# Kernel tuning notes

Hardware: AMD Instinct MI355X
Metric: run time of the kernel (lower is better)

The kernel has to match this reference:

```python
import jax, jax.numpy as jnp
import numpy as np

B, T, C = 4, 2048, 1024
H = 16
HS = C // H  # 64

def setup_inputs() -> dict:
    key = jax.random.key(0)
    k1, k2, k3, k4 = jax.random.split(key, 4)
    scale = 0.02
    return {
        "x": jax.random.normal(k1, (B, T, C), dtype=jnp.float32),
        "w_kqv": jax.random.normal(k2, (C, 3 * C), dtype=jnp.float32) * scale,
        "w_proj": jax.random.normal(k3, (C, C), dtype=jnp.float32) * scale,
        "b_proj": jax.random.normal(k4, (C,), dtype=jnp.float32) * scale,
    }

def reference(x, w_kqv, w_proj, b_proj):
    b, t, c = x.shape
    qkv = x @ w_kqv                       # [B,T,3C]
    q, k, v = jnp.split(qkv, 3, axis=-1)
    def heads(a):
        return a.reshape(b, t, H, HS).transpose(0, 2, 1, 3)  # [B,H,T,HS]
    q, k, v = heads(q), heads(k), heads(v)
    # faithful to source: scores MULTIPLIED by sqrt(head_size)
    scores = jnp.einsum('bhqd,bhkd->bhqk', q, k) * (HS ** 0.5)
    mask = jnp.tril(jnp.ones((t, t), dtype=bool))
    scores = jnp.where(mask[None, None], scores, -jnp.inf)
    attn = jax.nn.softmax(scores, axis=-1)
    out = jnp.einsum('bhqk,bhkd->bhqd', attn, v)  # [B,H,T,HS]
    out = out.transpose(0, 2, 1, 3).reshape(b, t, c)
    return out @ w_proj + b_proj
```

## Files before the change

kernel.cpp:

```cpp
#include <hip/hip_runtime.h>
#include <hip/hip_bf16.h>
#include <cstdint>

#define BB 4
#define TT 2048
#define CC 1024
#define HH 16
#define HS 64
#define MM (BB*TT)

#define QSCALE 11.5415603629f

typedef _Float16 f16;
typedef _Float16 f16x8 __attribute__((ext_vector_type(8)));
typedef _Float16 f16x4 __attribute__((ext_vector_type(4)));
typedef float f32x4 __attribute__((ext_vector_type(4)));
typedef float f32x16 __attribute__((ext_vector_type(16)));

#define MFMA16(a,b,c) __builtin_amdgcn_mfma_f32_16x16x32_f16(a,b,c,0,0,0)
#define MFMA32(a,b,c) __builtin_amdgcn_mfma_f32_32x32x16_f16(a,b,c,0,0,0)

__device__ __forceinline__ void g2lds16(void* lds, const void* g) {
  __builtin_amdgcn_global_load_lds(
      (const __attribute__((address_space(1))) void*)g,
      (__attribute__((address_space(3))) void*)lds, 16, 0, 0);
}

__device__ __forceinline__ int pk2(float a, float b) {
  auto r = __builtin_amdgcn_cvt_pkrtz(a, b);
  return __builtin_bit_cast(int, r);
}

union U8 { int4 i; f16x8 h; };

__global__ __launch_bounds__(256) void cvt_kernel(const float* __restrict__ in,
                                                  f16* __restrict__ out, int n4) {
  int i = blockIdx.x * blockDim.x + threadIdx.x;
  if (i < n4) {
    float4 v = ((const float4*)in)[i];
    f16x4 o;
    o[0] = (f16)v.x; o[1] = (f16)v.y; o[2] = (f16)v.z; o[3] = (f16)v.w;
    ((f16x4*)out)[i] = o;
  }
}

__global__ __launch_bounds__(256) void transpose_cvt(const float* __restrict__ in,
                                                     f16* __restrict__ out,
                                                     int K, int N) {
  __shared__ float tile[32][33];
  int n0 = blockIdx.x * 32, k0 = blockIdx.y * 32;
  int tx = threadIdx.x, ty = threadIdx.y;
  #pragma unroll
  for (int i = 0; i < 32; i += 8)
    tile[ty + i][tx] = in[(size_t)(k0 + ty + i) * N + n0 + tx];
  __syncthreads();
  #pragma unroll
  for (int i = 0; i < 32; i += 8)
    out[(size_t)(n0 + ty + i) * K + k0 + tx] = (f16)tile[tx][ty + i];
}

__device__ __forceinline__ void gstage(const f16* __restrict__ A,
                                       const f16* __restrict__ Bt,
                                       f16* as, f16* bs,
                                       int row0, int col0, int kt, int t) {
  const int K = 1024;
  #pragma unroll
  for (int i = 0; i < 2; ++i) {
    int off = i * 8192 + t * 16;
    int row = off >> 7;
    int cbB = off & 127;
    int scb = cbB ^ ((row & 7) << 4);
    g2lds16((char*)as + off, (const char*)(A  + (size_t)(row0 + row) * K + kt) + scb);
    g2lds16((char*)bs + off, (const char*)(Bt + (size_t)(col0 + row) * K + kt) + scb);
  }
}

template<int EPI>
__global__ __launch_bounds__(512) void gemm_bt(const f16* __restrict__ A,
                                               const f16* __restrict__ Bt,
                                               f16* __restrict__ qT,
                                               f16* __restrict__ kT,
                                               f16* __restrict__ vT,
                                               const float* __restrict__ bias,
                                               float* __restrict__ outF) {
  const int K = 1024;
  __shared__ f16 As[2][128 * 64];
  __shared__ f16 Bs[2][128 * 64];
  const int t = threadIdx.x;
  const int l = t & 63, w = t >> 6;
  const int lr = l & 15, lh = l >> 4;
  const int row0 = blockIdx.y * 128, col0 = blockIdx.x * 128;
  const int wm = w >> 2, wn = w & 3;
  const int wr = wm * 64, wc = wn * 32;
  const int sx = (lr & 7) << 4;

  f32x4 acc[4][2] = {};

  gstage(A, Bt, As[0], Bs[0], row0, col0, 0, t);
  int buf = 0;
  for (int kt = 0; kt < K; kt += 64) {
    asm volatile("" ::: "memory");
    const bool pf = (kt + 64) < K;
    if (pf) gstage(A, Bt, As[buf ^ 1], Bs[buf ^ 1], row0, col0, kt + 64, t);
    if (pf) asm volatile("s_waitcnt vmcnt(4)" ::: "memory");
    else    asm volatile("s_waitcnt vmcnt(0)" ::: "memory");
    __builtin_amdgcn_sched_barrier(0);
    __builtin_amdgcn_s_barrier();
    const char* as = (const char*)As[buf];
    const char* bs = (const char*)Bs[buf];
    __builtin_amdgcn_s_setprio(1);
    #pragma unroll
    for (int kk = 0; kk < 64; kk += 32) {
      f16x8 af[4], bfr[2];
      #pragma unroll
      for (int m = 0; m < 4; ++m)
        af[m]  = *(const f16x8*)(as + (wr + m * 16 + lr) * 128
                                    + ((kk * 2 + lh * 16) ^ sx));
      #pragma unroll
      for (int n = 0; n < 2; ++n)
        bfr[n] = *(const f16x8*)(bs + (wc + n * 16 + lr) * 128
                                    + ((kk * 2 + lh * 16) ^ sx));
      #pragma unroll
      for (int m = 0; m < 4; ++m)
        #pragma unroll
        for (int n = 0; n < 2; ++n)
          acc[m][n] = MFMA16(af[m], bfr[n], acc[m][n]);
    }
    __builtin_amdgcn_s_setprio(0);
    __builtin_amdgcn_sched_barrier(0);
    __builtin_amdgcn_s_barrier();
    buf ^= 1;
  }

  #pragma unroll
  for (int m = 0; m < 4; ++m) {
    #pragma unroll
    for (int n = 0; n < 2; ++n) {
      #pragma unroll
      for (int j = 0; j < 4; ++j) {
        float val = acc[m][n][j];
        int gr = row0 + wr + m * 16 + lh * 4 + j;
        int gc = col0 + wc + n * 16 + lr;
        if (EPI == 0) {
          int which = gc >> 10;
          int c = gc & 1023;
          int h = c >> 6, d = c & 63;
          int b = gr >> 11, tt = gr & 2047;
          size_t bh = (size_t)(b * HH + h);
          if (which == 0)      qT[(bh * TT + tt) * HS + d] = (f16)(val * QSCALE);
          else if (which == 1) kT[(bh * TT + tt) * HS + d] = (f16)val;
          else                 vT[(bh * HS + d) * TT + tt] = (f16)val;
        } else {
          outF[(size_t)gr * CC + gc] = val + bias[gc];
        }
      }
    }
  }
}

template<bool MASKED>
__device__ __forceinline__ void step32L(
    int kglob, int qa, int l31, int hi,
    const f16* __restrict__ ks, const f16* __restrict__ vs, int kbs,
    const f16x8 (&qf)[4],
    float& m, f32x4& lv, f32x16& oA, f32x16& oB) {
  const int sx = (l31 & 7) << 4;
  const char* krow = (const char*)(ks + (kbs + l31) * 64);
  f32x16 s = {};
  #pragma unroll
  for (int j = 0; j < 4; ++j) {
    f16x8 kf = *(const f16x8*)(krow + ((j * 32 + hi * 16) ^ sx));
    s = MFMA32(kf, qf[j], s);
  }
  float p[16];
  #pragma unroll
  for (int r = 0; r < 16; ++r) {
    if (MASKED) {
      int k = kglob + (r & 3) + 8 * (r >> 2) + 4 * hi;
      p[r] = (k <= qa) ? s[r] : -INFINITY;
    } else p[r] = s[r];
  }
  float t0 = fmaxf(fmaxf(p[0], p[1]), fmaxf(p[2], p[3]));
  float t1 = fmaxf(fmaxf(p[4], p[5]), fmaxf(p[6], p[7]));
  float t2 = fmaxf(fmaxf(p[8], p[9]), fmaxf(p[10], p[11]));
  float t3 = fmaxf(fmaxf(p[12], p[13]), fmaxf(p[14], p[15]));
  float mx = fmaxf(fmaxf(t0, t1), fmaxf(t2, t3));
  if (__any(mx > m + 14.0f)) {
    mx = fmaxf(mx, __shfl_xor(mx, 32));
    float mn = fmaxf(m, mx);
    float corr = __builtin_amdgcn_exp2f(m - mn);
    m = mn;
    #pragma unroll
    for (int r = 0; r < 4; ++r) lv[r] *= corr;
    #pragma unroll
    for (int r = 0; r < 16; ++r) { oA[r] *= corr; oB[r] *= corr; }
  }
  #pragma unroll
  for (int r = 0; r < 16; ++r) {
    p[r] = __builtin_amdgcn_exp2f(p[r] - m);
    lv[r & 3] += p[r];
  }
  int pk[8], xk[8];
  #pragma unroll
  for (int j = 0; j < 8; ++j) pk[j] = pk2(p[2 * j], p[2 * j + 1]);
  #pragma unroll
  for (int j = 0; j < 8; ++j) xk[j] = __shfl_xor(pk[j], 32);
  U8 b0, b1;
  b0.i = (int4){ hi ? xk[2] : pk[0], hi ? xk[3] : pk[1],
                 hi ? pk[2] : xk[0], hi ? pk[3] : xk[1] };
  b1.i = (int4){ hi ? xk[6] : pk[4], hi ? xk[7] : pk[5],
                 hi ? pk[6] : xk[4], hi ? pk[7] : xk[5] };
  const char* vrow0 = (const char*)(vs + l31 * 64);
  const char* vrow1 = (const char*)(vs + (l31 + 32) * 64);
  const int kc0 = (kbs * 2 + hi * 16) ^ sx;
  const int kc1 = (kbs * 2 + hi * 16 + 32) ^ sx;
  f16x8 v00 = *(const f16x8*)(vrow0 + kc0);
  f16x8 v01 = *(const f16x8*)(vrow0 + kc1);
  f16x8 v10 = *(const f16x8*)(vrow1 + kc0);
  f16x8 v11 = *(const f16x8*)(vrow1 + kc1);
  oA = MFMA32(v00, b0.h, oA);
  oA = MFMA32(v01, b1.h, oA);
  oB = MFMA32(v10, b0.h, oB);
  oB = MFMA32(v11, b1.h, oB);
}

__device__ __forceinline__ void stage_tile(const f16* __restrict__ Kb,
                                           const f16* __restrict__ Vb,
                                           f16* ks, f16* vs,
                                           int kb, int w, int l) {
  #pragma unroll
  for (int j = 0; j < 2; ++j) {
    int off = w * 2048 + j * 1024 + l * 16;
    int row = off >> 7;
    int cb  = off & 127;
    int scb = cb ^ ((row & 7) << 4);
    g2lds16((char*)ks + off, (const char*)(Kb + (size_t)(kb + row) * HS) + scb);
    g2lds16((char*)vs + off, (const char*)(Vb + (size_t)row * TT + kb) + scb);
  }
}

__global__ __launch_bounds__(256) void attn_kernel(const f16* __restrict__ qT,
                                                   const f16* __restrict__ kT,
                                                   const f16* __restrict__ vT,
                                                   f16* __restrict__ aout) {
  const int bh = blockIdx.x;
  const int pr = blockIdx.y;
  const int t = threadIdx.x, l = t & 63, w = t >> 6;
  const int l31 = l & 31, hi = l >> 5;
  const f16* __restrict__ Qb = qT + (size_t)bh * TT * HS;
  const f16* __restrict__ Kb = kT + (size_t)bh * TT * HS;
  const f16* __restrict__ Vb = vT + (size_t)bh * HS * TT;
  const int b = bh >> 4, h = bh & 15;

  __shared__ f16 Ks[2][64 * 64];
  __shared__ f16 Vs[2][64 * 64];

  #pragma unroll
  for (int ph = 0; ph < 2; ++ph) {
    const int qb = ph ? pr : (15 - pr);
    const int q0w = qb * 128 + w * 32;
    const int qa = q0w + l31;

    f16x8 qf[4];
    #pragma unroll
    for (int j = 0; j < 4; ++j)
      qf[j] = *(const f16x8*)&Qb[(size_t)qa * HS + 16 * j + hi * 8];

    float m = -INFINITY;
    f32x4 lv = {};
    f32x16 oA = {}, oB = {};

    const int nt = 2 * qb + 2;
    stage_tile(Kb, Vb, Ks[0], Vs[0], 0, w, l);
    __syncthreads();
    int buf = 0;
    for (int ti = 0; ti < nt; ++ti) {
      if (ti + 1 < nt)
        stage_tile(Kb, Vb, Ks[buf ^ 1], Vs[buf ^ 1], (ti + 1) * 64, w, l);
      const int kb = ti * 64;
      const f16* ks = Ks[buf];
      const f16* vs = Vs[buf];
      if (kb < q0w)
        step32L<false>(kb, qa, l31, hi, ks, vs, 0, qf, m, lv, oA, oB);
      else if (kb == q0w)
        step32L<true >(kb, qa, l31, hi, ks, vs, 0, qf, m, lv, oA, oB);
      if (kb + 32 < q0w)
        step32L<false>(kb + 32, qa, l31, hi, ks, vs, 32, qf, m, lv, oA, oB);
      else if (kb + 32 == q0w)
        step32L<true >(kb + 32, qa, l31, hi, ks, vs, 32, qf, m, lv, oA, oB);
      __syncthreads();
      buf ^= 1;
    }

    float lsum = (lv[0] + lv[1]) + (lv[2] + lv[3]);
    lsum += __shfl_xor(lsum, 32);
    float li = 1.0f / lsum;

    f16* orow = aout + (size_t)(b * TT + qa) * CC + h * HS;
    #pragma unroll
    for (int rq = 0; rq < 4; ++rq) {
      f16x4 o4a, o4b;
      #pragma unroll
      for (int j = 0; j < 4; ++j) {
        int r = rq * 4 + j;
        o4a[j] = (f16)(oA[r] * li);
        o4b[j] = (f16)(oB[r] * li);
      }
      int dA = 8 * rq + 4 * hi;
      *(f16x4*)&orow[dA]      = o4a;
      *(f16x4*)&orow[32 + dA] = o4b;
    }
    __syncthreads();
  }
}

extern "C" void kernel_launch(void* const* d_in, const int* in_sizes, int n_in,
                              void* d_out, int out_size, void* d_ws, size_t ws_size,
                              hipStream_t stream) {
  const float* x      = (const float*)d_in[0];
  const float* w_kqv  = (const float*)d_in[1];
  const float* w_proj = (const float*)d_in[2];
  const float* b_proj = (const float*)d_in[3];
  float* out = (float*)d_out;

  char* ws = (char*)d_ws;
  f16* xb    = (f16*)(ws);
  f16* wkqvT = (f16*)(ws + 16777216);
  f16* wpT   = (f16*)(ws + 23068672);
  f16* qT    = (f16*)(ws + 25165824);
  f16* kT    = (f16*)(ws + 41943040);
  f16* vT    = (f16*)(ws + 58720256);
  f16* aout  = (f16*)(ws + 75497472);

  cvt_kernel<<<8192, 256, 0, stream>>>(x, xb, (MM * CC) / 4);
  transpose_cvt<<<dim3(3 * CC / 32, CC / 32), dim3(32, 8), 0, stream>>>(w_kqv, wkqvT, CC, 3 * CC);
  transpose_cvt<<<dim3(CC / 32, CC / 32), dim3(32, 8), 0, stream>>>(w_proj, wpT, CC, CC);

  gemm_bt<0><<<dim3(3 * CC / 128, MM / 128), 512, 0, stream>>>(xb, wkqvT, qT, kT, vT, nullptr, nullptr);

  attn_kernel<<<dim3(BB * HH, 8), 256, 0, stream>>>(qT, kT, vT, aout);

  gemm_bt<1><<<dim3(CC / 128, MM / 128), 512, 0, stream>>>(aout, wpT, nullptr, nullptr, nullptr, b_proj, out);
}
```

Before: 211.4 us.

## Halve GEMM K-tile with paired-row LDS layout and split QK^T MFMA chains

The projection GEMM now stages a 32-wide K slice per iteration instead of 64. It uses a new LDS layout that packs two rows per 128-byte line with a different XOR swizzle. This halves LDS use per block, which may allow more blocks per CU, at the cost of twice as many loop iterations and barriers. Separately, the attention QK^T score computation splits its four dependent MFMAs into two independent accumulator chains summed afterwards, to shorten the MFMA dependency chain.

```diff
diff --git a/kernel.cpp b/kernel.cpp
--- a/kernel.cpp
+++ b/kernel.cpp
@@ -64,15 +64,11 @@
                                        f16* as, f16* bs,
                                        int row0, int col0, int kt, int t) {
   const int K = 1024;
-  #pragma unroll
-  for (int i = 0; i < 2; ++i) {
-    int off = i * 8192 + t * 16;
-    int row = off >> 7;
-    int cbB = off & 127;
-    int scb = cbB ^ ((row & 7) << 4);
-    g2lds16((char*)as + off, (const char*)(A  + (size_t)(row0 + row) * K + kt) + scb);
-    g2lds16((char*)bs + off, (const char*)(Bt + (size_t)(col0 + row) * K + kt) + scb);
-  }
+  int off = t * 16;
+  int row = ((off >> 7) << 1) | ((off >> 6) & 1);
+  int cb  = (off & 63) ^ (((off >> 7) & 3) << 4);
+  g2lds16((char*)as + off, (const char*)(A  + (size_t)(row0 + row) * K + kt) + cb);
+  g2lds16((char*)bs + off, (const char*)(Bt + (size_t)(col0 + row) * K + kt) + cb);
 }
 
 template<int EPI>
@@ -84,42 +80,44 @@
                                                const float* __restrict__ bias,
                                                float* __restrict__ outF) {
   const int K = 1024;
-  __shared__ f16 As[2][128 * 64];
-  __shared__ f16 Bs[2][128 * 64];
+  __shared__ f16 As[2][128 * 32];
+  __shared__ f16 Bs[2][128 * 32];
   const int t = threadIdx.x;
   const int l = t & 63, w = t >> 6;
   const int lr = l & 15, lh = l >> 4;
   const int row0 = blockIdx.y * 128, col0 = blockIdx.x * 128;
   const int wm = w >> 2, wn = w & 3;
   const int wr = wm * 64, wc = wn * 32;
-  const int sx = (lr & 7) << 4;
+  const int sx2 = (lh * 16) ^ ((((lr >> 1) & 3)) << 4);
+  const int rodd = (lr & 1) * 64;
 
   f32x4 acc[4][2] = {};
 
   gstage(A, Bt, As[0], Bs[0], row0, col0, 0, t);
   int buf = 0;
-  for (int kt = 0; kt < K; kt += 64) {
+  for (int kt = 0; kt < K; kt += 32) {
     asm volatile("" ::: "memory");
-    const bool pf = (kt + 64) < K;
-    if (pf) gstage(A, Bt, As[buf ^ 1], Bs[buf ^ 1], row0, col0, kt + 64, t);
-    if (pf) asm volatile("s_waitcnt vmcnt(4)" ::: "memory");
+    const bool pf = (kt + 32) < K;
+    if (pf) gstage(A, Bt, As[buf ^ 1], Bs[buf ^ 1], row0, col0, kt + 32, t);
+    if (pf) asm volatile("s_waitcnt vmcnt(2)" ::: "memory");
     else    asm volatile("s_waitcnt vmcnt(0)" ::: "memory");
     __builtin_amdgcn_sched_barrier(0);
     __builtin_amdgcn_s_barrier();
     const char* as = (const char*)As[buf];
     const char* bs = (const char*)Bs[buf];
     __builtin_amdgcn_s_setprio(1);
-    #pragma unroll
-    for (int kk = 0; kk < 64; kk += 32) {
+    {
       f16x8 af[4], bfr[2];
       #pragma unroll
-      for (int m = 0; m < 4; ++m)
-        af[m]  = *(const f16x8*)(as + (wr + m * 16 + lr) * 128
-                                    + ((kk * 2 + lh * 16) ^ sx));
-      #pragma unroll
-      for (int n = 0; n < 2; ++n)
-        bfr[n] = *(const f16x8*)(bs + (wc + n * 16 + lr) * 128
-                                    + ((kk * 2 + lh * 16) ^ sx));
+      for (int m = 0; m < 4; ++m) {
+        int p = (wr >> 1) + m * 8 + (lr >> 1);
+        af[m]  = *(const f16x8*)(as + p * 128 + rodd + sx2);
+      }
+      #pragma unroll
+      for (int n = 0; n < 2; ++n) {
+        int p = (wc >> 1) + n * 8 + (lr >> 1);
+        bfr[n] = *(const f16x8*)(bs + p * 128 + rodd + sx2);
+      }
       #pragma unroll
       for (int m = 0; m < 4; ++m)
         #pragma unroll
@@ -166,19 +164,25 @@
     float& m, f32x4& lv, f32x16& oA, f32x16& oB) {
   const int sx = (l31 & 7) << 4;
   const char* krow = (const char*)(ks + (kbs + l31) * 64);
-  f32x16 s = {};
-  #pragma unroll
-  for (int j = 0; j < 4; ++j) {
-    f16x8 kf = *(const f16x8*)(krow + ((j * 32 + hi * 16) ^ sx));
-    s = MFMA32(kf, qf[j], s);
+  f32x16 sa = {}, sb = {};
+  {
+    f16x8 kf0 = *(const f16x8*)(krow + ((0 * 32 + hi * 16) ^ sx));
+    f16x8 kf1 = *(const f16x8*)(krow + ((1 * 32 + hi * 16) ^ sx));
+    f16x8 kf2 = *(const f16x8*)(krow + ((2 * 32 + hi * 16) ^ sx));
+    f16x8 kf3 = *(const f16x8*)(krow + ((3 * 32 + hi * 16) ^ sx));
+    sa = MFMA32(kf0, qf[0], sa);
+    sb = MFMA32(kf2, qf[2], sb);
+    sa = MFMA32(kf1, qf[1], sa);
+    sb = MFMA32(kf3, qf[3], sb);
   }
   float p[16];
   #pragma unroll
   for (int r = 0; r < 16; ++r) {
+    float sv = sa[r] + sb[r];
     if (MASKED) {
       int k = kglob + (r & 3) + 8 * (r >> 2) + 4 * hi;
-      p[r] = (k <= qa) ? s[r] : -INFINITY;
-    } else p[r] = s[r];
+      p[r] = (k <= qa) ? sv : -INFINITY;
+    } else p[r] = sv;
   }
   float t0 = fmaxf(fmaxf(p[0], p[1]), fmaxf(p[2], p[3]));
   float t1 = fmaxf(fmaxf(p[4], p[5]), fmaxf(p[6], p[7]));
```

After: 233.7 us. +10.6%, slower.
